# Kernel tuning notes

Measured on AMD Instinct MI355X. Metric: run time of the kernel, lower is better.

## Reference

```python
import jax, jax.numpy as jnp
import numpy as np

B, L, H, NH = 1, 4096, 768, 12
HD = H // NH  # 64


def setup_inputs() -> dict:
    key = jax.random.key(0)
    ks = jax.random.split(key, 10)
    inp = {
        "query": jax.random.normal(ks[0], (B, L, H), jnp.float32),
        "key": jax.random.normal(ks[1], (B, L, H), jnp.float32),
        "value": jax.random.normal(ks[2], (B, L, H), jnp.float32),
        "attention_mask": jnp.zeros((B, 1, 1, L), jnp.float32),
        # learned params (nn.Linear: y = x @ W.T + b)
        "Wq": jax.random.normal(ks[3], (H, H), jnp.float32) * 0.02,
        "bq": jnp.zeros((H,), jnp.float32),
        "Wk": jax.random.normal(ks[4], (H, H), jnp.float32) * 0.02,
        "bk": jnp.zeros((H,), jnp.float32),
        "Wv": jax.random.normal(ks[5], (H, H), jnp.float32) * 0.02,
        "bv": jnp.zeros((H,), jnp.float32),
    }
    return inp


def _split_heads(x):
    # [B, L, H] -> [B, NH, L, HD]
    b, l, _ = x.shape
    return x.reshape(b, l, NH, HD).transpose(0, 2, 1, 3)


def reference(query, key, value, attention_mask, Wq, bq, Wk, bk, Wv, bv):
    q = _split_heads(query @ Wq.T + bq)   # [B, NH, Lq, HD]
    k = _split_heads(key @ Wk.T + bk)     # [B, NH, Lk, HD]
    v = _split_heads(value @ Wv.T + bv)   # [B, NH, Lk, HD]

    scale = 1.0 / jnp.sqrt(jnp.asarray(HD, q.dtype))
    scores = jnp.einsum("bhqd,bhkd->bhqk", q, k) * scale
    scores = scores + attention_mask  # additive mask, broadcasts over heads/queries
    probs = jax.nn.softmax(scores, axis=-1)
    # dropout is identity in eval mode (reference baseline)
    ctx = jnp.einsum("bhqk,bhkd->bhqd", probs, v)  # [B, NH, Lq, HD]
    out = ctx.transpose(0, 2, 1, 3).reshape(query.shape[0], query.shape[1], H)
    return out
```

## Files before the change

kernel.cpp:

```cpp
#include <hip/hip_runtime.h>
#include <math.h>

#define LSEQ 4096
#define HDIM 768
#define NHEAD 12

using v4f    = __attribute__((ext_vector_type(4))) float;
using short8 = __attribute__((ext_vector_type(8))) short;
using u32x4  = __attribute__((ext_vector_type(4))) unsigned int;

#if __has_builtin(__builtin_amdgcn_exp2f)
#define EXP2F(x) __builtin_amdgcn_exp2f(x)
#else
#define EXP2F(x) exp2f(x)
#endif

#define GLOAD_LDS16(g, l)                                                  \
  __builtin_amdgcn_global_load_lds(                                       \
      (const __attribute__((address_space(1))) unsigned int*)(g),         \
      (__attribute__((address_space(3))) unsigned int*)(l), 16, 0, 0)

__device__ __forceinline__ unsigned short f2bf(float f) {
  union { float f; unsigned u; } v; v.f = f;
  unsigned r = v.u + 0x7fffu + ((v.u >> 16) & 1u);
  return (unsigned short)(r >> 16);
}

__device__ __forceinline__ short8 cvt8(u32x4 a, u32x4 b) {
  short8 r;
#pragma unroll
  for (int i = 0; i < 4; ++i) {
    unsigned u = a[i];
    r[i] = (short)((u + 0x7fffu + ((u >> 16) & 1u)) >> 16);
  }
#pragma unroll
  for (int i = 0; i < 4; ++i) {
    unsigned u = b[i];
    r[4 + i] = (short)((u + 0x7fffu + ((u >> 16) & 1u)) >> 16);
  }
  return r;
}

__global__ __launch_bounds__(256, 2) void proj_gemm(
    const float* __restrict__ Xq, const float* __restrict__ Xk,
    const float* __restrict__ Xv,
    const float* __restrict__ Wq, const float* __restrict__ Wk,
    const float* __restrict__ Wv,
    const float* __restrict__ bq, const float* __restrict__ bk,
    const float* __restrict__ bv,
    unsigned short* __restrict__ dst_base)
{
  __shared__ __align__(16) unsigned short a_lds[128 * 32];
  __shared__ __align__(16) unsigned short b_lds[128 * 32];
  __shared__ __align__(16) unsigned short c_lds[64 * 136];

  const int id = blockIdx.x;
  const int xcd = id & 7, local = id >> 3;
  const int grp = local / 6, bnIdx = local % 6;
  const int G = grp * 8 + xcd;
  const int z = G >> 5;
  const int bm = (G & 31) * 128, bn = bnIdx * 128;

  const float* X = (z == 0) ? Xq : ((z == 1) ? Xk : Xv);
  const float* W = (z == 0) ? Wq : ((z == 1) ? Wk : Wv);
  const float* bias = (z == 0) ? bq : ((z == 1) ? bk : bv);
  unsigned short* dst = dst_base + (size_t)z * NHEAD * LSEQ * 64;

  const int tid = threadIdx.x;
  const int wave = tid >> 6, lane = tid & 63;
  const int quad = lane >> 4, l16 = lane & 15;
  const int wm = (wave >> 1) * 64, wn = (wave & 1) * 64;

  v4f acc[4][4];
  for (int i = 0; i < 4; ++i)
    for (int j = 0; j < 4; ++j)
      acc[i][j] = (v4f){0.f, 0.f, 0.f, 0.f};

  const int row_s = tid >> 2;
  const int c8_s = (tid & 3) * 8;

  const float* xrow[2]; const float* wrow[2];
#pragma unroll
  for (int s = 0; s < 2; ++s) {
    xrow[s] = X + (size_t)(bm + row_s + 64 * s) * HDIM + c8_s;
    wrow[s] = W + (size_t)(bn + row_s + 64 * s) * HDIM + c8_s;
  }

  u32x4 pa[2][2], pb[2][2];
#pragma unroll
  for (int s = 0; s < 2; ++s) {
    pa[s][0] = *(const u32x4*)(xrow[s]);     pa[s][1] = *(const u32x4*)(xrow[s] + 4);
    pb[s][0] = *(const u32x4*)(wrow[s]);     pb[s][1] = *(const u32x4*)(wrow[s] + 4);
  }

  for (int k0 = 0; k0 < HDIM; k0 += 32) {
    __syncthreads();
#pragma unroll
    for (int s = 0; s < 2; ++s) {
      *(short8*)&a_lds[(row_s + 64 * s) * 32 + c8_s] = cvt8(pa[s][0], pa[s][1]);
      *(short8*)&b_lds[(row_s + 64 * s) * 32 + c8_s] = cvt8(pb[s][0], pb[s][1]);
    }
    __syncthreads();

    if (k0 + 32 < HDIM) {
#pragma unroll
      for (int s = 0; s < 2; ++s) {
        pa[s][0] = *(const u32x4*)(xrow[s] + k0 + 32);
        pa[s][1] = *(const u32x4*)(xrow[s] + k0 + 36);
        pb[s][0] = *(const u32x4*)(wrow[s] + k0 + 32);
        pb[s][1] = *(const u32x4*)(wrow[s] + k0 + 36);
      }
    }

    short8 af[4], bfr[4];
    for (int i = 0; i < 4; ++i)
      af[i] = *(const short8*)&a_lds[(wm + i * 16 + l16) * 32 + quad * 8];
    for (int j = 0; j < 4; ++j)
      bfr[j] = *(const short8*)&b_lds[(wn + j * 16 + l16) * 32 + quad * 8];
    if (z == 2) {
      for (int i = 0; i < 4; ++i)
        for (int j = 0; j < 4; ++j)
          acc[i][j] = __builtin_amdgcn_mfma_f32_16x16x32_bf16(bfr[j], af[i], acc[i][j], 0, 0, 0);
    } else {
      for (int i = 0; i < 4; ++i)
        for (int j = 0; j < 4; ++j)
          acc[i][j] = __builtin_amdgcn_mfma_f32_16x16x32_bf16(af[i], bfr[j], acc[i][j], 0, 0, 0);
    }
  }

  for (int p = 0; p < 2; ++p) {
    __syncthreads();
    if (z == 2) {
      if ((wave & 1) == p) {
        for (int j = 0; j < 4; ++j)
          for (int r = 0; r < 4; ++r) {
            float bvv = bias[bn + wn + j * 16 + quad * 4 + r];
            int row = j * 16 + quad * 4 + r;
            for (int i = 0; i < 4; ++i)
              c_lds[row * 136 + wm + i * 16 + l16] = f2bf(acc[i][j][r] + bvv);
          }
      }
    } else {
      if ((wave >> 1) == p) {
        for (int j = 0; j < 4; ++j) {
          float bvv = bias[bn + wn + j * 16 + l16];
          for (int i = 0; i < 4; ++i)
            for (int r = 0; r < 4; ++r)
              c_lds[(i * 16 + quad * 4 + r) * 136 + wn + j * 16 + l16] =
                  f2bf(acc[i][j][r] + bvv);
        }
      }
    }
    __syncthreads();
    int row = tid >> 2, c = tid & 3;
    const unsigned short* srow = &c_lds[row * 136 + c * 32];
    if (z == 2) {
      int n = bn + p * 64 + row;
      int hh = n >> 6, d = n & 63;
      unsigned short* drow = dst + ((size_t)hh * 64 + d) * LSEQ + bm + c * 32;
      for (int q8 = 0; q8 < 4; ++q8)
        *(u32x4*)(drow + q8 * 8) = *(const u32x4*)(srow + q8 * 8);
    } else {
      int m = bm + p * 64 + row;
      int nbase = bn + c * 32;
      int hh = nbase >> 6, d = nbase & 63;
      unsigned short* drow = dst + ((size_t)hh * LSEQ + m) * 64 + d;
      for (int q8 = 0; q8 < 4; ++q8)
        *(u32x4*)(drow + q8 * 8) = *(const u32x4*)(srow + q8 * 8);
    }
  }
}

__global__ __launch_bounds__(256, 3) void attn(
    const unsigned short* __restrict__ Q, const unsigned short* __restrict__ K,
    const unsigned short* __restrict__ Vt, const float* __restrict__ mask,
    float* __restrict__ out)
{
  __shared__ __align__(16) unsigned short k_lds[2][64 * 64];
  __shared__ __align__(16) unsigned short vt_lds[2][64 * 64];
  __shared__ __align__(16) unsigned short p_lds[4][32 * 64];
  __shared__ float lsum_lds[2][32];

  const int h = blockIdx.y;
  const int qt = blockIdx.x;
  const int tid = threadIdx.x;
  const int wave = tid >> 6, lane = tid & 63;
  const int quad = lane >> 4, l16 = lane & 15;
  const int qg = wave & 1, kh = wave >> 1;

  const unsigned short* Qh  = Q  + (size_t)h * LSEQ * 64;
  const unsigned short* Kh  = K  + (size_t)h * LSEQ * 64;
  const unsigned short* Vth = Vt + (size_t)h * 64 * LSEQ;

  const unsigned short* ksrc[2]; const unsigned short* vsrc[2];
  unsigned short* kdst[2]; unsigned short* vdst[2];
#pragma unroll
  for (int s = 0; s < 2; ++s) {
    int seg = wave * 2 + s;
    int rl = lane >> 3, cc = (lane & 7) ^ rl;
    ksrc[s] = Kh + (size_t)(seg * 8 + rl) * 64 + cc * 8;
    vsrc[s] = Vth + (size_t)(seg * 8 + rl) * LSEQ + cc * 8;
    kdst[s] = &k_lds[0][seg * 512];
    vdst[s] = &vt_lds[0][seg * 512];
  }

  short8 qf[2][2];
#pragma unroll
  for (int i = 0; i < 2; ++i)
#pragma unroll
    for (int c = 0; c < 2; ++c)
      qf[i][c] = *(const short8*)(Qh + (size_t)(qt * 64 + qg * 32 + i * 16 + l16) * 64 +
                                  c * 32 + quad * 8);

  int pswzR[2];
#pragma unroll
  for (int i = 0; i < 2; ++i) {
    int rr = i * 16 + l16;
    pswzR[i] = (rr ^ (rr >> 2)) & 7;
  }

  short8 ones;
#pragma unroll
  for (int i = 0; i < 8; ++i) ones[i] = (short)0x3F80;

  v4f acc_o[2][4];
#pragma unroll
  for (int i = 0; i < 2; ++i)
    for (int j = 0; j < 4; ++j) acc_o[i][j] = (v4f){0.f, 0.f, 0.f, 0.f};
  v4f acc_l[2];
  acc_l[0] = (v4f){0.f, 0.f, 0.f, 0.f};
  acc_l[1] = (v4f){0.f, 0.f, 0.f, 0.f};

#pragma unroll
  for (int s = 0; s < 2; ++s) { GLOAD_LDS16(ksrc[s], kdst[s]); GLOAD_LDS16(vsrc[s], vdst[s]); }

  for (int kt = 0; kt < 64; ++kt) {
    const int key0 = kt * 64;
    const int buf = kt & 1, nbuf = (kt + 1) & 1;

    __syncthreads();

    if (kt < 63) {
      size_t ko = (size_t)(key0 + 64) * 64;
#pragma unroll
      for (int s = 0; s < 2; ++s) {
        GLOAD_LDS16(ksrc[s] + ko, kdst[s] + nbuf * 4096);
        GLOAD_LDS16(vsrc[s] + (key0 + 64), vdst[s] + nbuf * 4096);
      }
    }

    float mk[2];
#pragma unroll
    for (int kg = 0; kg < 2; ++kg)
      mk[kg] = mask[key0 + kh * 32 + kg * 16 + l16] * 1.44269504f;

    v4f sacc[2][2];
#pragma unroll
    for (int i = 0; i < 2; ++i)
      for (int kg = 0; kg < 2; ++kg) sacc[i][kg] = (v4f){0.f, 0.f, 0.f, 0.f};
#pragma unroll
    for (int c = 0; c < 2; ++c)
#pragma unroll
      for (int kg = 0; kg < 2; ++kg) {
        int row = kh * 32 + kg * 16 + l16;
        short8 kf = *(const short8*)&k_lds[buf][row * 64 + (((c * 4 + quad) ^ (row & 7)) << 3)];
#pragma unroll
        for (int i = 0; i < 2; ++i)
          sacc[i][kg] = __builtin_amdgcn_mfma_f32_16x16x32_bf16(qf[i][c], kf, sacc[i][kg], 0, 0, 0);
      }

#pragma unroll
    for (int i = 0; i < 2; ++i)
#pragma unroll
      for (int kg = 0; kg < 2; ++kg)
#pragma unroll
        for (int r = 0; r < 4; ++r) {
          union { float f; unsigned u; } pu;
          pu.f = EXP2F(fmaf(sacc[i][kg][r], 0.18033688f, mk[kg]));
          int prow = i * 16 + quad * 4 + r;
          int col = kg * 16 + l16;
          int swz = (prow ^ (prow >> 2)) & 7;
          p_lds[wave][prow * 64 + (((col >> 3) ^ swz) << 3) + (col & 7)] =
              (unsigned short)(pu.u >> 16);
        }
    short8 pf[2];
#pragma unroll
    for (int i = 0; i < 2; ++i)
      pf[i] = *(const short8*)&p_lds[wave][(i * 16 + l16) * 64 + (((quad ^ pswzR[i]) & 7) << 3)];

    short8 vfj[4];
#pragma unroll
    for (int j = 0; j < 4; ++j) {
      int d = j * 16 + l16;
      vfj[j] = *(const short8*)&vt_lds[buf][d * 64 + (((kh * 4 + quad) ^ (d & 7)) << 3)];
    }
#pragma unroll
    for (int i = 0; i < 2; ++i) {
#pragma unroll
      for (int j = 0; j < 4; ++j)
        acc_o[i][j] = __builtin_amdgcn_mfma_f32_16x16x32_bf16(pf[i], vfj[j], acc_o[i][j], 0, 0, 0);
      acc_l[i] = __builtin_amdgcn_mfma_f32_16x16x32_bf16(pf[i], ones, acc_l[i], 0, 0, 0);
    }
  }

  __syncthreads();
  float* merge = (float*)&p_lds[0][0];
  if (kh == 1) {
#pragma unroll
    for (int i = 0; i < 2; ++i) {
#pragma unroll
      for (int j = 0; j < 4; ++j)
#pragma unroll
        for (int r = 0; r < 4; ++r)
          merge[qg * 2048 + (i * 16 + quad * 4 + r) * 64 + j * 16 + l16] = acc_o[i][j][r];
      if (l16 == 0)
#pragma unroll
        for (int r = 0; r < 4; ++r)
          lsum_lds[qg][i * 16 + quad * 4 + r] = acc_l[i][r];
    }
  }
  __syncthreads();
  if (kh == 0) {
#pragma unroll
    for (int i = 0; i < 2; ++i) {
      float den[4];
#pragma unroll
      for (int r = 0; r < 4; ++r)
        den[r] = acc_l[i][r] + lsum_lds[qg][i * 16 + quad * 4 + r];
#pragma unroll
      for (int j = 0; j < 4; ++j) {
        int col = h * 64 + j * 16 + l16;
#pragma unroll
        for (int r = 0; r < 4; ++r) {
          int row = qt * 64 + qg * 32 + i * 16 + quad * 4 + r;
          float o = acc_o[i][j][r] +
                    merge[qg * 2048 + (i * 16 + quad * 4 + r) * 64 + j * 16 + l16];
          out[(size_t)row * HDIM + col] = o / den[r];
        }
      }
    }
  }
}

extern "C" void kernel_launch(void* const* d_in, const int* in_sizes, int n_in,
                              void* d_out, int out_size, void* d_ws, size_t ws_size,
                              hipStream_t stream) {
  const float* query = (const float*)d_in[0];
  const float* key   = (const float*)d_in[1];
  const float* value = (const float*)d_in[2];
  const float* mask  = (const float*)d_in[3];
  const float* Wq = (const float*)d_in[4];
  const float* bq = (const float*)d_in[5];
  const float* Wk = (const float*)d_in[6];
  const float* bk = (const float*)d_in[7];
  const float* Wv = (const float*)d_in[8];
  const float* bv = (const float*)d_in[9];
  float* out = (float*)d_out;

  unsigned short* Qb = (unsigned short*)d_ws;
  unsigned short* Kb = Qb + (size_t)NHEAD * LSEQ * 64;
  unsigned short* Vb = Kb + (size_t)NHEAD * LSEQ * 64;

  proj_gemm<<<576, 256, 0, stream>>>(
      query, key, value, Wq, Wk, Wv, bq, bk, bv, Qb);
  attn<<<dim3(LSEQ / 64, NHEAD), 256, 0, stream>>>(Qb, Kb, Vb, mask, out);
}
```

Baseline: 228.3 us.

## Keep P in registers via transposed MFMA, drop LDS round-trip and ones-MFMA

```diff
diff --git a/kernel.cpp b/kernel.cpp
--- a/kernel.cpp
+++ b/kernel.cpp
@@ -6,6 +6,7 @@
 #define NHEAD 12
 
 using v4f    = __attribute__((ext_vector_type(4))) float;
+using f4     = __attribute__((ext_vector_type(4))) float;
 using short8 = __attribute__((ext_vector_type(8))) short;
 using u32x4  = __attribute__((ext_vector_type(4))) unsigned int;
 
@@ -136,8 +137,10 @@
           for (int r = 0; r < 4; ++r) {
             float bvv = bias[bn + wn + j * 16 + quad * 4 + r];
             int row = j * 16 + quad * 4 + r;
-            for (int i = 0; i < 4; ++i)
-              c_lds[row * 136 + wm + i * 16 + l16] = f2bf(acc[i][j][r] + bvv);
+            for (int i = 0; i < 4; ++i) {
+              int colp = wm + (i >> 1) * 32 + (l16 >> 2) * 8 + (i & 1) * 4 + (l16 & 3);
+              c_lds[row * 136 + colp] = f2bf(acc[i][j][r] + bvv);
+            }
           }
       }
     } else {
@@ -176,10 +179,7 @@
     const unsigned short* __restrict__ Vt, const float* __restrict__ mask,
     float* __restrict__ out)
 {
-  __shared__ __align__(16) unsigned short k_lds[2][64 * 64];
-  __shared__ __align__(16) unsigned short vt_lds[2][64 * 64];
-  __shared__ __align__(16) unsigned short p_lds[4][32 * 64];
-  __shared__ float lsum_lds[2][32];
+  __shared__ __align__(16) unsigned short smem[4 * 64 * 64];
 
   const int h = blockIdx.y;
   const int qt = blockIdx.x;
@@ -200,36 +200,23 @@
     int rl = lane >> 3, cc = (lane & 7) ^ rl;
     ksrc[s] = Kh + (size_t)(seg * 8 + rl) * 64 + cc * 8;
     vsrc[s] = Vth + (size_t)(seg * 8 + rl) * LSEQ + cc * 8;
-    kdst[s] = &k_lds[0][seg * 512];
-    vdst[s] = &vt_lds[0][seg * 512];
+    kdst[s] = smem + seg * 512;
+    vdst[s] = smem + 8192 + seg * 512;
   }
 
   short8 qf[2][2];
 #pragma unroll
-  for (int i = 0; i < 2; ++i)
+  for (int qi = 0; qi < 2; ++qi)
 #pragma unroll
     for (int c = 0; c < 2; ++c)
-      qf[i][c] = *(const short8*)(Qh + (size_t)(qt * 64 + qg * 32 + i * 16 + l16) * 64 +
-                                  c * 32 + quad * 8);
-
-  int pswzR[2];
-#pragma unroll
-  for (int i = 0; i < 2; ++i) {
-    int rr = i * 16 + l16;
-    pswzR[i] = (rr ^ (rr >> 2)) & 7;
-  }
-
-  short8 ones;
-#pragma unroll
-  for (int i = 0; i < 8; ++i) ones[i] = (short)0x3F80;
-
-  v4f acc_o[2][4];
-#pragma unroll
-  for (int i = 0; i < 2; ++i)
-    for (int j = 0; j < 4; ++j) acc_o[i][j] = (v4f){0.f, 0.f, 0.f, 0.f};
-  v4f acc_l[2];
-  acc_l[0] = (v4f){0.f, 0.f, 0.f, 0.f};
-  acc_l[1] = (v4f){0.f, 0.f, 0.f, 0.f};
+      qf[qi][c] = *(const short8*)(Qh + (size_t)(qt * 64 + qg * 32 + qi * 16 + l16) * 64 +
+                                   c * 32 + quad * 8);
+
+  v4f acc[2][4];
+#pragma unroll
+  for (int qi = 0; qi < 2; ++qi)
+    for (int j = 0; j < 4; ++j) acc[qi][j] = (v4f){0.f, 0.f, 0.f, 0.f};
+  float lsum[2] = {0.f, 0.f};
 
 #pragma unroll
   for (int s = 0; s < 2; ++s) { GLOAD_LDS16(ksrc[s], kdst[s]); GLOAD_LDS16(vsrc[s], vdst[s]); }
@@ -249,94 +236,105 @@
       }
     }
 
-    float mk[2];
-#pragma unroll
-    for (int kg = 0; kg < 2; ++kg)
-      mk[kg] = mask[key0 + kh * 32 + kg * 16 + l16] * 1.44269504f;
+    f4 mv[2];
+#pragma unroll
+    for (int k2 = 0; k2 < 2; ++k2)
+      mv[k2] = *(const f4*)(mask + key0 + kh * 32 + k2 * 16 + quad * 4);
+
+    const unsigned short* kb = smem + buf * 4096;
+    short8 kf[2][2];
+#pragma unroll
+    for (int k2 = 0; k2 < 2; ++k2)
+#pragma unroll
+      for (int c = 0; c < 2; ++c) {
+        int row = kh * 32 + k2 * 16 + l16;
+        kf[k2][c] = *(const short8*)&kb[row * 64 + (((c * 4 + quad) ^ (row & 7)) << 3)];
+      }
 
     v4f sacc[2][2];
 #pragma unroll
-    for (int i = 0; i < 2; ++i)
-      for (int kg = 0; kg < 2; ++kg) sacc[i][kg] = (v4f){0.f, 0.f, 0.f, 0.f};
+    for (int k2 = 0; k2 < 2; ++k2)
+      for (int qi = 0; qi < 2; ++qi) sacc[k2][qi] = (v4f){0.f, 0.f, 0.f, 0.f};
 #pragma unroll
     for (int c = 0; c < 2; ++c)
 #pragma unroll
-      for (int kg = 0; kg < 2; ++kg) {
-        int row = kh * 32 + kg * 16 + l16;
-        short8 kf = *(const short8*)&k_lds[buf][row * 64 + (((c * 4 + quad) ^ (row & 7)) << 3)];
-#pragma unroll
-        for (int i = 0; i < 2; ++i)
-          sacc[i][kg] = __builtin_amdgcn_mfma_f32_16x16x32_bf16(qf[i][c], kf, sacc[i][kg], 0, 0, 0);
-      }
-
-#pragma unroll
-    for (int i = 0; i < 2; ++i)
-#pragma unroll
-      for (int kg = 0; kg < 2; ++kg)
+      for (int k2 = 0; k2 < 2; ++k2)
+#pragma unroll
+        for (int qi = 0; qi < 2; ++qi)
+          sacc[k2][qi] = __builtin_amdgcn_mfma_f32_16x16x32_bf16(
+              kf[k2][c], qf[qi][c], sacc[k2][qi], 0, 0, 0);
+
+    union { unsigned u[4]; short8 s8; } pb[2];
+#pragma unroll
+    for (int qi = 0; qi < 2; ++qi)
+#pragma unroll
+      for (int k2 = 0; k2 < 2; ++k2) {
+        unsigned pu[4];
 #pragma unroll
         for (int r = 0; r < 4; ++r) {
-          union { float f; unsigned u; } pu;
-          pu.f = EXP2F(fmaf(sacc[i][kg][r], 0.18033688f, mk[kg]));
-          int prow = i * 16 + quad * 4 + r;
-          int col = kg * 16 + l16;
-          int swz = (prow ^ (prow >> 2)) & 7;
-          p_lds[wave][prow * 64 + (((col >> 3) ^ swz) << 3) + (col & 7)] =
-              (unsigned short)(pu.u >> 16);
+          union { float f; unsigned u; } t;
+          t.f = EXP2F(fmaf(sacc[k2][qi][r], 0.18033688f, mv[k2][r] * 1.44269504f));
+          t.u &= 0xffff0000u;
+          lsum[qi] += t.f;
+          pu[r] = t.u;
         }
-    short8 pf[2];
-#pragma unroll
-    for (int i = 0; i < 2; ++i)
-      pf[i] = *(const short8*)&p_lds[wave][(i * 16 + l16) * 64 + (((quad ^ pswzR[i]) & 7) << 3)];
-
-    short8 vfj[4];
+        pb[qi].u[k2 * 2 + 0] = (pu[0] >> 16) | (pu[1] & 0xffff0000u);
+        pb[qi].u[k2 * 2 + 1] = (pu[2] >> 16) | (pu[3] & 0xffff0000u);
+      }
+
+    const unsigned short* vb = smem + 8192 + buf * 4096;
+    short8 vf[4];
 #pragma unroll
     for (int j = 0; j < 4; ++j) {
       int d = j * 16 + l16;
-      vfj[j] = *(const short8*)&vt_lds[buf][d * 64 + (((kh * 4 + quad) ^ (d & 7)) << 3)];
-    }
-#pragma unroll
-    for (int i = 0; i < 2; ++i) {
+      vf[j] = *(const short8*)&vb[d * 64 + (((kh * 4 + quad) ^ (d & 7)) << 3)];
+    }
+
+#pragma unroll
+    for (int qi = 0; qi < 2; ++qi)
 #pragma unroll
       for (int j = 0; j < 4; ++j)
-        acc_o[i][j] = __builtin_amdgcn_mfma_f32_16x16x32_bf16(pf[i], vfj[j], acc_o[i][j], 0, 0, 0);
-      acc_l[i] = __builtin_amdgcn_mfma_f32_16x16x32_bf16(pf[i], ones, acc_l[i], 0, 0, 0);
-    }
+        acc[qi][j] = __builtin_amdgcn_mfma_f32_16x16x32_bf16(
+            vf[j], pb[qi].s8, acc[qi][j], 0, 0, 0);
+  }
+
+#pragma unroll
+  for (int qi = 0; qi < 2; ++qi) {
+    float l = lsum[qi];
+    l += __shfl_xor(l, 16, 64);
+    l += __shfl_xor(l, 32, 64);
+    lsum[qi] = l;
   }
 
   __syncthreads();
-  float* merge = (float*)&p_lds[0][0];
+  float* mrg = (float*)smem;
+  float* lsl = mrg + 64 * 66;
   if (kh == 1) {
 #pragma unroll
-    for (int i = 0; i < 2; ++i) {
+    for (int qi = 0; qi < 2; ++qi) {
+      int qrow = (qg * 2 + qi) * 16 + l16;
 #pragma unroll
       for (int j = 0; j < 4; ++j)
 #pragma unroll
         for (int r = 0; r < 4; ++r)
-          merge[qg * 2048 + (i * 16 + quad * 4 + r) * 64 + j * 16 + l16] = acc_o[i][j][r];
-      if (l16 == 0)
-#pragma unroll
-        for (int r = 0; r < 4; ++r)
-          lsum_lds[qg][i * 16 + quad * 4 + r] = acc_l[i][r];
+          mrg[qrow * 66 + j * 16 + quad * 4 + r] = acc[qi][j][r];
+      if (quad == 0) lsl[qrow] = lsum[qi];
     }
   }
   __syncthreads();
   if (kh == 0) {
 #pragma unroll
-    for (int i = 0; i < 2; ++i) {
-      float den[4];
-#pragma unroll
-      for (int r = 0; r < 4; ++r)
-        den[r] = acc_l[i][r] + lsum_lds[qg][i * 16 + quad * 4 + r];
+    for (int qi = 0; qi < 2; ++qi) {
+      int qrow = (qg * 2 + qi) * 16 + l16;
+      float inv = 1.0f / (lsum[qi] + lsl[qrow]);
+      int row = qt * 64 + qg * 32 + qi * 16 + l16;
 #pragma unroll
       for (int j = 0; j < 4; ++j) {
-        int col = h * 64 + j * 16 + l16;
-#pragma unroll
-        for (int r = 0; r < 4; ++r) {
-          int row = qt * 64 + qg * 32 + i * 16 + quad * 4 + r;
-          float o = acc_o[i][j][r] +
-                    merge[qg * 2048 + (i * 16 + quad * 4 + r) * 64 + j * 16 + l16];
-          out[(size_t)row * HDIM + col] = o / den[r];
-        }
+        f4 o;
+#pragma unroll
+        for (int r = 0; r < 4; ++r)
+          o[r] = (acc[qi][j][r] + mrg[qrow * 66 + j * 16 + quad * 4 + r]) * inv;
+        *(f4*)(out + (size_t)row * HDIM + h * 64 + j * 16 + quad * 4) = o;
       }
     }
   }
```

Result: faster. 219.2 us (-4.0%).
